# Kernel tuning notes

Hardware: AMD Instinct MI355X
Metric: run time of the kernel (lower is better)

## Reference

```python
import jax, jax.numpy as jnp
import numpy as np

L, B, E, H, NL = 512, 8, 1024, 16, 2
HD = E // H
DFF = 4 * E
EPS = 1e-5


def setup_inputs() -> dict:
    key = jax.random.key(0)
    ks = jax.random.split(key, 8)
    s = 0.02
    return {
        "src": jax.random.normal(ks[0], (L, B, E), jnp.float32),
        "position_embed": jax.random.normal(ks[1], (L, L, HD), jnp.float32) * s,
        "type_embed": jax.random.normal(ks[2], (L, L, HD), jnp.float32) * s,
        "Wi": jax.random.normal(ks[3], (NL, 3 * E, E), jnp.float32) * s,
        "bi": jnp.zeros((NL, 3 * E), jnp.float32),
        "Wo": jax.random.normal(ks[4], (NL, E, E), jnp.float32) * s,
        "bo": jnp.zeros((NL, E), jnp.float32),
        "W1": jax.random.normal(ks[5], (NL, DFF, E), jnp.float32) * s,
        "b1": jnp.zeros((NL, DFF), jnp.float32),
        "W2": jax.random.normal(ks[6], (NL, E, DFF), jnp.float32) * s,
        "b2": jnp.zeros((NL, E), jnp.float32),
        "g1": jnp.ones((NL, E), jnp.float32),
        "be1": jnp.zeros((NL, E), jnp.float32),
        "g2": jnp.ones((NL, E), jnp.float32),
        "be2": jnp.zeros((NL, E), jnp.float32),
    }


def _ln(x, g, b):
    m = jnp.mean(x, -1, keepdims=True)
    v = jnp.mean((x - m) ** 2, -1, keepdims=True)
    return (x - m) * jax.lax.rsqrt(v + EPS) * g + b


def _attn(src, pos, typ, Wi, bi, Wo, bo):
    # src: [L, B, E]
    p = src @ Wi.T + bi                      # [L, B, 3E]
    q, k, v = jnp.split(p, 3, axis=-1)
    q = q * (HD ** -0.5)
    # -> [B, H, L, HD]
    def hsplit(t):
        return t.reshape(L, B, H, HD).transpose(1, 2, 0, 3)
    q, k, v = hsplit(q), hsplit(k), hsplit(v)
    # scores = q k^T + type_embed@q + q@pos^T  (Shaw relative attention)
    scores = jnp.einsum('bhld,bhsd->bhls', q, k)
    scores = scores + jnp.einsum('bhld,lsd->bhls', q, pos)      # position term
    scores = scores + jnp.einsum('lsd,bhld->bhls', typ, q)      # type term
    w = jax.nn.softmax(scores, axis=-1)                          # [B, H, L, S]
    # output = w v + w@pos + typ^T@w
    out = jnp.einsum('bhls,bhsd->bhld', w, v)
    out = out + jnp.einsum('bhls,lsd->bhld', w, pos)
    out = out + jnp.einsum('bhls,lsd->bhld', w, typ)
    out = out.transpose(2, 0, 1, 3).reshape(L, B, E)            # [L, B, E]
    return out @ Wo.T + bo


def _layer(src, pos, typ, Wi, bi, Wo, bo, W1, b1, W2, b2, g1, be1, g2, be2):
    src2 = _attn(src, pos, typ, Wi, bi, Wo, bo)
    src = _ln(src + src2, g1, be1)
    h = jax.nn.gelu(src @ W1.T + b1, approximate=False)
    src2 = h @ W2.T + b2
    return _ln(src + src2, g2, be2)


def reference(src, position_embed, type_embed, Wi, bi, Wo, bo, W1, b1, W2, b2,
              g1, be1, g2, be2):
    out = src
    for i in range(NL):
        out = _layer(out, position_embed, type_embed,
                     Wi[i], bi[i], Wo[i], bo[i], W1[i], b1[i], W2[i], b2[i],
                     g1[i], be1[i], g2[i], be2[i])
    return out
```

## Files before the change

kernel.cpp:

```cpp
#include <hip/hip_runtime.h>
#include <hip/hip_bf16.h>
#include <math.h>


typedef __hip_bfloat16 bf16;
typedef short short8 __attribute__((ext_vector_type(8)));
typedef float f32x4 __attribute__((ext_vector_type(4)));

typedef __attribute__((address_space(1))) const void gvoid;
typedef __attribute__((address_space(3))) void lvoid;

constexpr int Lc = 512;
constexpr int Bc = 8;
constexpr int Ec = 1024;
constexpr int Hc = 16;
constexpr int HDc = 64;
constexpr int NLc = 2;
constexpr int DFFc = 4096;
constexpr int LB = Lc * Bc;
constexpr int BHc = Bc * Hc;
constexpr float EPSc = 1e-5f;

__device__ inline unsigned short f2bfu(float f) {
  union { __hip_bfloat16 h; unsigned short u; } cv;
  cv.h = __float2bfloat16(f);
  return cv.u;
}

template <bool ACC, bool GELU, bool OBF>
__global__ __launch_bounds__(256) void gemm_bt128d(
    int M, int N, int K,
    const bf16* __restrict__ A, int lda, long long sAz,
    const bf16* __restrict__ Bm, int ldb, long long sBz,
    void* __restrict__ Cv, int ldc, long long sCz,
    const float* __restrict__ bias) {
  __shared__ __align__(16) bf16 As[2 * 128 * 64];
  __shared__ __align__(16) bf16 Bs[2 * 128 * 64];
  const int tid = threadIdx.x;
  const int w = tid >> 6, lane = tid & 63, quad = lane >> 4, lr = lane & 15;
  const int wr = w >> 1, wc = w & 1;
  const int m0 = blockIdx.x * 128, n0 = blockIdx.y * 128;
  const long long z = blockIdx.z;
  A += z * sAz;
  Bm += z * sBz;
  float* Cf = (float*)Cv;
  bf16* Cb = (bf16*)Cv;

  f32x4 acc[4][4];
#pragma unroll
  for (int i = 0; i < 4; i++)
#pragma unroll
    for (int j = 0; j < 4; j++) acc[i][j] = {0.f, 0.f, 0.f, 0.f};

  const int rA = lane >> 3;
  const int cA = ((lane & 7) ^ (lane >> 3)) * 8;

  auto STAGE = [&](int buf, int kt) {
    const int k0 = kt << 6;
#pragma unroll
    for (int t = 0; t < 4; ++t) {
      const int chunk = w * 4 + t;
      const int row = chunk * 8 + rA;
      __builtin_amdgcn_global_load_lds(
          (gvoid*)(A + (long long)(m0 + row) * lda + k0 + cA),
          (lvoid*)(As + buf * 8192 + chunk * 512), 16, 0, 0);
      __builtin_amdgcn_global_load_lds(
          (gvoid*)(Bm + (long long)(n0 + row) * ldb + k0 + cA),
          (lvoid*)(Bs + buf * 8192 + chunk * 512), 16, 0, 0);
    }
  };

  auto LOAD = [&](int buf, short8 (&a)[2][4], short8 (&b)[2][4]) {
    const char* Ab = (const char*)(As + buf * 8192);
    const char* Bb = (const char*)(Bs + buf * 8192);
#pragma unroll
    for (int ks2 = 0; ks2 < 2; ks2++) {
      const int swzc = (ks2 * 64 + quad * 16) ^ ((lr & 7) << 4);
#pragma unroll
      for (int i = 0; i < 4; i++)
        a[ks2][i] = *(const short8*)(Ab + (wr * 64 + i * 16 + lr) * 128 + swzc);
#pragma unroll
      for (int j = 0; j < 4; j++)
        b[ks2][j] = *(const short8*)(Bb + (wc * 64 + j * 16 + lr) * 128 + swzc);
    }
  };

  auto MMA = [&](short8 (&a)[2][4], short8 (&b)[2][4]) {
#pragma unroll
    for (int ks2 = 0; ks2 < 2; ks2++)
#pragma unroll
      for (int i = 0; i < 4; i++)
#pragma unroll
        for (int j = 0; j < 4; j++)
          acc[i][j] = __builtin_amdgcn_mfma_f32_16x16x32_bf16(a[ks2][i], b[ks2][j], acc[i][j], 0, 0, 0);
  };

  const int nt = K >> 6;
  STAGE(0, 0);
  asm volatile("s_waitcnt vmcnt(0)" ::: "memory");
  __builtin_amdgcn_sched_barrier(0);
  __builtin_amdgcn_s_barrier();
  __builtin_amdgcn_sched_barrier(0);

  int cur = 0;
  for (int t = 0; t < nt - 1; ++t) {
    short8 a[2][4], b[2][4];
    LOAD(cur, a, b);
    __builtin_amdgcn_sched_barrier(0);
    STAGE(cur ^ 1, t + 1);
    __builtin_amdgcn_sched_barrier(0);
    __builtin_amdgcn_s_setprio(1);
    MMA(a, b);
    __builtin_amdgcn_s_setprio(0);
    asm volatile("s_waitcnt vmcnt(0)" ::: "memory");
    __builtin_amdgcn_sched_barrier(0);
    __builtin_amdgcn_s_barrier();
    __builtin_amdgcn_sched_barrier(0);
    cur ^= 1;
  }
  {
    short8 a[2][4], b[2][4];
    LOAD(cur, a, b);
    MMA(a, b);
  }

#pragma unroll
  for (int i = 0; i < 4; i++) {
#pragma unroll
    for (int j = 0; j < 4; j++) {
      int col = n0 + wc * 64 + j * 16 + lr;
      float bv = bias ? bias[col] : 0.f;
#pragma unroll
      for (int r = 0; r < 4; r++) {
        int row = m0 + wr * 64 + i * 16 + quad * 4 + r;
        long long off = z * sCz + (long long)row * ldc + col;
        float v = acc[i][j][r] + bv;
        if (ACC) v += Cf[off];
        if (GELU) v = 0.5f * v * (1.f + erff(v * 0.70710678118654752f));
        if (OBF)
          Cb[off] = __float2bfloat16(v);
        else
          Cf[off] = v;
      }
    }
  }
}

template <bool ACC, bool GELU, bool OBF>
__global__ __launch_bounds__(256) void gemm_bt(
    int M, int N, int K,
    const bf16* __restrict__ A, int lda, long long sAz,
    const bf16* __restrict__ Bm, int ldb, long long sBz,
    void* __restrict__ Cv, int ldc, long long sCz,
    const float* __restrict__ bias) {
  __shared__ __align__(16) bf16 As[128 * 72];
  __shared__ __align__(16) bf16 Bs[64 * 72];
  const int tid = threadIdx.x;
  const int w = tid >> 6, lane = tid & 63, quad = lane >> 4, lr = lane & 15;
  const int m0 = blockIdx.x * 128, n0 = blockIdx.y * 64;
  const long long z = blockIdx.z;
  A += z * sAz;
  Bm += z * sBz;
  float* Cf = (float*)Cv;
  bf16* Cb = (bf16*)Cv;

  f32x4 acc[2][4];
#pragma unroll
  for (int i = 0; i < 2; i++)
#pragma unroll
    for (int j = 0; j < 4; j++) acc[i][j] = {0.f, 0.f, 0.f, 0.f};

  for (int k0 = 0; k0 < K; k0 += 64) {
#pragma unroll
    for (int i = 0; i < 8; i++) {
      int slot = tid + i * 256;
      int r = slot >> 4, c4 = (slot & 15) << 2;
      const bf16* srcp = A + (long long)(m0 + r) * lda + k0 + c4;
      *(ushort4*)&As[r * 72 + c4] = *(const ushort4*)srcp;
    }
#pragma unroll
    for (int i = 0; i < 4; i++) {
      int slot = tid + i * 256;
      int r = slot >> 4, c4 = (slot & 15) << 2;
      const bf16* srcp = Bm + (long long)(n0 + r) * ldb + k0 + c4;
      *(ushort4*)&Bs[r * 72 + c4] = *(const ushort4*)srcp;
    }
    __syncthreads();
#pragma unroll
    for (int ks = 0; ks < 64; ks += 32) {
      short8 a[2], b[4];
#pragma unroll
      for (int i = 0; i < 2; i++)
        a[i] = *(const short8*)&As[(w * 32 + i * 16 + lr) * 72 + ks + quad * 8];
#pragma unroll
      for (int j = 0; j < 4; j++)
        b[j] = *(const short8*)&Bs[(j * 16 + lr) * 72 + ks + quad * 8];
#pragma unroll
      for (int i = 0; i < 2; i++)
#pragma unroll
        for (int j = 0; j < 4; j++)
          acc[i][j] = __builtin_amdgcn_mfma_f32_16x16x32_bf16(a[i], b[j], acc[i][j], 0, 0, 0);
    }
    __syncthreads();
  }

#pragma unroll
  for (int i = 0; i < 2; i++) {
#pragma unroll
    for (int j = 0; j < 4; j++) {
      int col = n0 + j * 16 + lr;
      float bv = bias ? bias[col] : 0.f;
#pragma unroll
      for (int r = 0; r < 4; r++) {
        int row = m0 + w * 32 + i * 16 + quad * 4 + r;
        long long off = z * sCz + (long long)row * ldc + col;
        float v = acc[i][j][r] + bv;
        if (ACC) v += Cf[off];
        if (GELU) v = 0.5f * v * (1.f + erff(v * 0.70710678118654752f));
        if (OBF)
          Cb[off] = __float2bfloat16(v);
        else
          Cf[off] = v;
      }
    }
  }
}

__global__ void cvt_bf16(const float* __restrict__ in, bf16* __restrict__ out, long long n) {
  long long i = (long long)blockIdx.x * 256 + threadIdx.x;
  if (i < n) out[i] = __float2bfloat16(in[i]);
}

__global__ void init_x(const float* __restrict__ src, float* __restrict__ x, bf16* __restrict__ xb) {
  long long i = (long long)blockIdx.x * 256 + threadIdx.x;
  float v = src[i];
  x[i] = v;
  xb[i] = __float2bfloat16(v);
}

__global__ void prep_R(const float* __restrict__ pos, const float* __restrict__ typ,
                       bf16* __restrict__ Rb, bf16* __restrict__ Rt) {
  __shared__ __align__(16) float Ls[64 * 68];
  int l = blockIdx.y, s0 = blockIdx.x * 64;
  int tid = threadIdx.x;
#pragma unroll
  for (int i = 0; i < 4; i++) {
    int slot = tid + i * 256;
    int r = slot >> 4, c = (slot & 15) << 2;
    long long off = (((long long)l) * Lc + s0 + r) * HDc + c;
    float4 a = *(const float4*)&pos[off];
    float4 b = *(const float4*)&typ[off];
    float4 s = {a.x + b.x, a.y + b.y, a.z + b.z, a.w + b.w};
    *(float4*)&Ls[r * 68 + c] = s;
    ushort4 o = {f2bfu(s.x), f2bfu(s.y), f2bfu(s.z), f2bfu(s.w)};
    *(ushort4*)&Rb[off] = o;
  }
  __syncthreads();
#pragma unroll
  for (int i = 0; i < 4; i++) {
    int slot = tid + i * 256;
    int d = slot >> 4, s4 = (slot & 15) << 2;
    ushort4 o = {f2bfu(Ls[(s4 + 0) * 68 + d]), f2bfu(Ls[(s4 + 1) * 68 + d]),
                 f2bfu(Ls[(s4 + 2) * 68 + d]), f2bfu(Ls[(s4 + 3) * 68 + d])};
    *(ushort4*)&Rt[(((long long)l) * HDc + d) * Lc + s0 + s4] = o;
  }
}

__global__ void split_qk(const float* __restrict__ P, bf16* __restrict__ q, bf16* __restrict__ k) {
  long long idx = (long long)blockIdx.x * 256 + threadIdx.x;
  int col = idx & (Ec - 1);
  long long row = idx >> 10;
  int l = (int)(row >> 3), b = (int)(row & 7);
  int h = col >> 6, d = col & 63;
  long long dst = (((long long)(b * Hc + h)) * Lc + l) * HDc + d;
  q[dst] = __float2bfloat16(P[row * 3072 + col] * 0.125f);
  k[dst] = __float2bfloat16(P[row * 3072 + Ec + col]);
}

__global__ void transpose_v(const float* __restrict__ P, bf16* __restrict__ vt) {
  __shared__ __align__(16) float Ls[64 * 68];
  int bh = blockIdx.y, b = bh >> 4, h = bh & 15;
  int l0 = blockIdx.x * 64;
  int tid = threadIdx.x;
#pragma unroll
  for (int i = 0; i < 4; i++) {
    int slot = tid + i * 256;
    int r = slot >> 4, c = (slot & 15) << 2;
    float4 v = *(const float4*)&P[((long long)(l0 + r) * Bc + b) * 3072 + 2 * Ec + h * 64 + c];
    *(float4*)&Ls[r * 68 + c] = v;
  }
  __syncthreads();
#pragma unroll
  for (int i = 0; i < 4; i++) {
    int slot = tid + i * 256;
    int d = slot >> 4, s4 = (slot & 15) << 2;
    ushort4 o = {f2bfu(Ls[(s4 + 0) * 68 + d]), f2bfu(Ls[(s4 + 1) * 68 + d]),
                 f2bfu(Ls[(s4 + 2) * 68 + d]), f2bfu(Ls[(s4 + 3) * 68 + d])};
    *(ushort4*)&vt[(((long long)(b * Hc + h)) * HDc + d) * Lc + l0 + s4] = o;
  }
}

__global__ __launch_bounds__(256) void softmax_rows(const float* S, bf16* P) {
  int w = threadIdx.x >> 6, lane = threadIdx.x & 63;
  long long row = (long long)blockIdx.x * 4 + w;
  const float* sr = S + row * 512;
  float4 v0 = *(const float4*)(sr + lane * 4);
  float4 v1 = *(const float4*)(sr + 256 + lane * 4);
  float mx = fmaxf(fmaxf(fmaxf(v0.x, v0.y), fmaxf(v0.z, v0.w)),
                   fmaxf(fmaxf(v1.x, v1.y), fmaxf(v1.z, v1.w)));
#pragma unroll
  for (int o = 32; o; o >>= 1) mx = fmaxf(mx, __shfl_xor(mx, o, 64));
  float e[8];
  e[0] = __expf(v0.x - mx); e[1] = __expf(v0.y - mx);
  e[2] = __expf(v0.z - mx); e[3] = __expf(v0.w - mx);
  e[4] = __expf(v1.x - mx); e[5] = __expf(v1.y - mx);
  e[6] = __expf(v1.z - mx); e[7] = __expf(v1.w - mx);
  float sum = e[0] + e[1] + e[2] + e[3] + e[4] + e[5] + e[6] + e[7];
#pragma unroll
  for (int o = 32; o; o >>= 1) sum += __shfl_xor(sum, o, 64);
  float inv = 1.f / sum;
  ushort4 o0 = {f2bfu(e[0] * inv), f2bfu(e[1] * inv), f2bfu(e[2] * inv), f2bfu(e[3] * inv)};
  ushort4 o1 = {f2bfu(e[4] * inv), f2bfu(e[5] * inv), f2bfu(e[6] * inv), f2bfu(e[7] * inv)};
  *(ushort4*)(P + row * 1024 + lane * 4) = o0;
  *(ushort4*)(P + row * 1024 + 256 + lane * 4) = o1;
}

__global__ void merge_ao(const float* __restrict__ ao2, bf16* __restrict__ aob) {
  long long i = (long long)blockIdx.x * 256 + threadIdx.x;
  int d = (int)(i & 63);
  long long t = i >> 6;
  int l = (int)(t & (Lc - 1));
  long long bh = t >> 9;
  int b = (int)(bh >> 4), h = (int)(bh & 15);
  aob[((long long)(l * Bc + b)) * Ec + h * 64 + d] = __float2bfloat16(ao2[i]);
}

__global__ __launch_bounds__(256) void add_ln4(
    const float* __restrict__ X, const float* __restrict__ Pp, long long pstride, int ns,
    const float* __restrict__ bias,
    const float* __restrict__ g, const float* __restrict__ be,
    float* __restrict__ outF, bf16* __restrict__ outB) {
  __shared__ float s_sum[4], s_sq[4];
  long long row = blockIdx.x;
  int tid = threadIdx.x;
  float4 xv = *(const float4*)&X[row * Ec + tid * 4];
  float4 bv = *(const float4*)&bias[tid * 4];
  float v[4] = {xv.x + bv.x, xv.y + bv.y, xv.z + bv.z, xv.w + bv.w};
  for (int s = 0; s < ns; ++s) {
    float4 pv = *(const float4*)&Pp[s * pstride + row * Ec + tid * 4];
    v[0] += pv.x; v[1] += pv.y; v[2] += pv.z; v[3] += pv.w;
  }
  float sm = v[0] + v[1] + v[2] + v[3];
  float sq = v[0] * v[0] + v[1] * v[1] + v[2] * v[2] + v[3] * v[3];
#pragma unroll
  for (int o = 32; o; o >>= 1) {
    sm += __shfl_xor(sm, o, 64);
    sq += __shfl_xor(sq, o, 64);
  }
  int w = tid >> 6, lane = tid & 63;
  if (lane == 0) {
    s_sum[w] = sm;
    s_sq[w] = sq;
  }
  __syncthreads();
  sm = s_sum[0] + s_sum[1] + s_sum[2] + s_sum[3];
  sq = s_sq[0] + s_sq[1] + s_sq[2] + s_sq[3];
  float mean = sm * (1.f / Ec);
  float var = sq * (1.f / Ec) - mean * mean;
  float rs = rsqrtf(var + EPSc);
#pragma unroll
  for (int e = 0; e < 4; e++) {
    int n = tid * 4 + e;
    float o = (v[e] - mean) * rs * g[n] + be[n];
    outF[row * Ec + n] = o;
    outB[row * Ec + n] = __float2bfloat16(o);
  }
}

static constexpr size_t WS_NEED = 327155712;

struct GlobalWs {
  void* p = nullptr;
  GlobalWs() {
    if (hipMalloc(&p, WS_NEED) != hipSuccess) p = nullptr;
  }
};
static GlobalWs g_ws;

extern "C" void kernel_launch(void* const* d_in, const int* in_sizes, int n_in,
                              void* d_out, int out_size, void* d_ws, size_t ws_size,
                              hipStream_t stream) {
  const float* src = (const float*)d_in[0];
  const float* pos = (const float*)d_in[1];
  const float* typ = (const float*)d_in[2];
  const float* Wi = (const float*)d_in[3];
  const float* bi = (const float*)d_in[4];
  const float* Wo = (const float*)d_in[5];
  const float* bo = (const float*)d_in[6];
  const float* W1 = (const float*)d_in[7];
  const float* b1 = (const float*)d_in[8];
  const float* W2 = (const float*)d_in[9];
  const float* b2 = (const float*)d_in[10];
  const float* g1 = (const float*)d_in[11];
  const float* be1 = (const float*)d_in[12];
  const float* g2 = (const float*)d_in[13];
  const float* be2 = (const float*)d_in[14];
  float* out = (float*)d_out;
  (void)in_sizes; (void)n_in; (void)out_size;

  char* wp = (ws_size >= WS_NEED) ? (char*)d_ws : (char*)g_ws.p;
  if (!wp) wp = (char*)d_ws;
  auto alloc = [&](size_t bytes) {
    char* r = wp;
    wp += (bytes + 255) & ~(size_t)255;
    return r;
  };

  char* U = alloc((size_t)BHc * Lc * Lc * 4);
  float* P = (float*)U;
  float* scores = (float*)U;
  bf16* probs = (bf16*)U;
  bf16* hb = (bf16*)U;
  float* part = (float*)(U + (size_t)34 * 1024 * 1024);
  const long long PSTRIDE = (long long)LB * Ec;

  float* x = (float*)alloc((size_t)LB * Ec * 4);
  bf16* xb = (bf16*)alloc((size_t)LB * Ec * 2);
  bf16* q = (bf16*)alloc((size_t)BHc * Lc * HDc * 2);
  bf16* k = (bf16*)alloc((size_t)BHc * Lc * HDc * 2);
  bf16* vt = (bf16*)alloc((size_t)BHc * HDc * Lc * 2);
  float* ao2 = (float*)alloc((size_t)BHc * Lc * HDc * 4);
  bf16* aob = (bf16*)alloc((size_t)LB * Ec * 2);
  bf16* Rb = (bf16*)alloc((size_t)Lc * Lc * HDc * 2);
  bf16* Rt = (bf16*)alloc((size_t)Lc * HDc * Lc * 2);
  bf16* wib = (bf16*)alloc((size_t)NLc * 3 * Ec * Ec * 2);
  bf16* wob = (bf16*)alloc((size_t)NLc * Ec * Ec * 2);
  bf16* w1b = (bf16*)alloc((size_t)NLc * DFFc * Ec * 2);
  bf16* w2b = (bf16*)alloc((size_t)NLc * Ec * DFFc * 2);

  {
    long long n;
    n = (long long)NLc * 3 * Ec * Ec;
    cvt_bf16<<<(int)((n + 255) / 256), 256, 0, stream>>>(Wi, wib, n);
    n = (long long)NLc * Ec * Ec;
    cvt_bf16<<<(int)((n + 255) / 256), 256, 0, stream>>>(Wo, wob, n);
    n = (long long)NLc * DFFc * Ec;
    cvt_bf16<<<(int)((n + 255) / 256), 256, 0, stream>>>(W1, w1b, n);
    n = (long long)NLc * Ec * DFFc;
    cvt_bf16<<<(int)((n + 255) / 256), 256, 0, stream>>>(W2, w2b, n);
  }
  prep_R<<<dim3(Lc / 64, Lc), 256, 0, stream>>>(pos, typ, Rb, Rt);
  init_x<<<LB * Ec / 256, 256, 0, stream>>>(src, x, xb);

  for (int i = 0; i < NLc; i++) {
    const bf16* Wi_b = wib + (size_t)i * 3 * Ec * Ec;
    const bf16* Wo_b = wob + (size_t)i * Ec * Ec;
    const bf16* W1_b = w1b + (size_t)i * DFFc * Ec;
    const bf16* W2_b = w2b + (size_t)i * Ec * DFFc;

    gemm_bt128d<false, false, false><<<dim3(LB / 128, 3 * Ec / 128, 1), 256, 0, stream>>>(
        LB, 3 * Ec, Ec, xb, Ec, 0, Wi_b, Ec, 0, P, 3 * Ec, 0, bi + (size_t)i * 3 * Ec);
    split_qk<<<LB * Ec / 256, 256, 0, stream>>>(P, q, k);
    transpose_v<<<dim3(Lc / 64, BHc), 256, 0, stream>>>(P, vt);

    gemm_bt<false, false, false><<<dim3(Lc / 128, Lc / 64, BHc), 256, 0, stream>>>(
        Lc, Lc, HDc, q, HDc, (long long)Lc * HDc, k, HDc, (long long)Lc * HDc,
        scores, Lc, (long long)Lc * Lc, nullptr);
    gemm_bt<true, false, false><<<dim3(1, Lc / 64, Lc), 256, 0, stream>>>(
        BHc, Lc, HDc, q, Lc * HDc, (long long)HDc, Rb, HDc, (long long)Lc * HDc,
        scores, Lc * Lc, (long long)Lc, nullptr);

    softmax_rows<<<BHc * Lc / 4, 256, 0, stream>>>(scores, probs);

    gemm_bt<false, false, false><<<dim3(Lc / 128, 1, BHc), 256, 0, stream>>>(
        Lc, HDc, Lc, probs, 1024, (long long)Lc * 1024, vt, Lc, (long long)HDc * Lc,
        ao2, HDc, (long long)Lc * HDc, nullptr);
    gemm_bt<true, false, false><<<dim3(1, 1, Lc), 256, 0, stream>>>(
        BHc, HDc, Lc, probs, Lc * 1024, (long long)1024, Rt, Lc, (long long)HDc * Lc,
        ao2, Lc * HDc, (long long)HDc, nullptr);

    merge_ao<<<BHc * Lc * HDc / 256, 256, 0, stream>>>(ao2, aob);

    gemm_bt128d<false, false, false><<<dim3(LB / 128, Ec / 128, 2), 256, 0, stream>>>(
        LB, Ec, Ec / 2, aob, Ec, (long long)(Ec / 2), Wo_b, Ec, (long long)(Ec / 2),
        part, Ec, PSTRIDE, nullptr);
    add_ln4<<<LB, 256, 0, stream>>>(x, part, PSTRIDE, 2, bo + (size_t)i * Ec,
                                    g1 + (size_t)i * Ec, be1 + (size_t)i * Ec, x, xb);

    gemm_bt128d<false, true, true><<<dim3(LB / 128, DFFc / 128, 1), 256, 0, stream>>>(
        LB, DFFc, Ec, xb, Ec, 0, W1_b, Ec, 0, hb, DFFc, 0, b1 + (size_t)i * DFFc);
    gemm_bt128d<false, false, false><<<dim3(LB / 128, Ec / 128, 2), 256, 0, stream>>>(
        LB, Ec, DFFc / 2, hb, DFFc, (long long)(DFFc / 2), W2_b, DFFc, (long long)(DFFc / 2),
        part, Ec, PSTRIDE, nullptr);

    float* outF = (i == NLc - 1) ? out : x;
    add_ln4<<<LB, 256, 0, stream>>>(x, part, PSTRIDE, 2, b2 + (size_t)i * Ec,
                                    g2 + (size_t)i * Ec, be2 + (size_t)i * Ec, outF, xb);
  }
}
```

Before: 1.097 ms.

## Fuse QK^T score GEMM into softmax kernel, reordering relative-term GEMM first

The separate q·k^T batched GEMM and the row softmax kernel are replaced by a single qk_softmax kernel. It computes the q·k^T tile with MFMA, adds the precomputed relative-position/type scores read from the scores buffer, and does the row max/sum reduction across four waves through shared memory before writing bf16 probabilities. The relative-term GEMM now writes (not accumulates) scores first. This removes one write plus re-read of the fp32 score tensor and one kernel launch. In exchange, q/k fragments are loaded straight from global memory without LDS staging, and extra block-level synchronisation is added.

```diff
diff --git a/kernel.cpp b/kernel.cpp
--- a/kernel.cpp
+++ b/kernel.cpp
@@ -5,6 +5,7 @@
 
 typedef __hip_bfloat16 bf16;
 typedef short short8 __attribute__((ext_vector_type(8)));
+typedef unsigned short ushort8 __attribute__((ext_vector_type(8)));
 typedef float f32x4 __attribute__((ext_vector_type(4)));
 
 typedef __attribute__((address_space(1))) const void gvoid;
@@ -226,6 +227,120 @@
   }
 }
 
+__global__ __launch_bounds__(256) void qk_softmax(
+    const bf16* __restrict__ q, const bf16* __restrict__ kk,
+    const float* S, bf16* Pr) {
+  __shared__ float red[4][32];
+  __shared__ __align__(16) unsigned short pbuf[32][520];
+  const int tid = threadIdx.x;
+  const int w = tid >> 6, lane = tid & 63, quad = lane >> 4, lr = lane & 15;
+  const int bh = blockIdx.z;
+  const int l0 = blockIdx.x * 32;
+  const int s0 = w * 128;
+  const long long qbase = (long long)bh * Lc * HDc;
+
+  f32x4 acc[2][8];
+#pragma unroll
+  for (int i = 0; i < 2; i++)
+#pragma unroll
+    for (int j = 0; j < 8; j++) acc[i][j] = {0.f, 0.f, 0.f, 0.f};
+
+#pragma unroll
+  for (int ks2 = 0; ks2 < 2; ks2++) {
+    short8 a[2], b[8];
+#pragma unroll
+    for (int i = 0; i < 2; i++)
+      a[i] = *(const short8*)&q[qbase + (long long)(l0 + i * 16 + lr) * HDc + ks2 * 32 + quad * 8];
+#pragma unroll
+    for (int j = 0; j < 8; j++)
+      b[j] = *(const short8*)&kk[qbase + (long long)(s0 + j * 16 + lr) * HDc + ks2 * 32 + quad * 8];
+#pragma unroll
+    for (int i = 0; i < 2; i++)
+#pragma unroll
+      for (int j = 0; j < 8; j++)
+        acc[i][j] = __builtin_amdgcn_mfma_f32_16x16x32_bf16(a[i], b[j], acc[i][j], 0, 0, 0);
+  }
+
+  const long long srow0 = (long long)bh * Lc + l0;
+#pragma unroll
+  for (int i = 0; i < 2; i++)
+#pragma unroll
+    for (int r = 0; r < 4; r++) {
+      const float* sp = S + (srow0 + i * 16 + quad * 4 + r) * Lc + s0 + lr;
+#pragma unroll
+      for (int j = 0; j < 8; j++) acc[i][j][r] += sp[j * 16];
+    }
+
+  float mx[2][4];
+#pragma unroll
+  for (int i = 0; i < 2; i++)
+#pragma unroll
+    for (int r = 0; r < 4; r++) {
+      float m = acc[i][0][r];
+#pragma unroll
+      for (int j = 1; j < 8; j++) m = fmaxf(m, acc[i][j][r]);
+#pragma unroll
+      for (int o = 8; o; o >>= 1) m = fmaxf(m, __shfl_xor(m, o, 64));
+      mx[i][r] = m;
+    }
+  if (lr == 0) {
+#pragma unroll
+    for (int i = 0; i < 2; i++)
+#pragma unroll
+      for (int r = 0; r < 4; r++) red[w][i * 16 + quad * 4 + r] = mx[i][r];
+  }
+  __syncthreads();
+#pragma unroll
+  for (int i = 0; i < 2; i++)
+#pragma unroll
+    for (int r = 0; r < 4; r++) {
+      int rr = i * 16 + quad * 4 + r;
+      mx[i][r] = fmaxf(fmaxf(red[0][rr], red[1][rr]), fmaxf(red[2][rr], red[3][rr]));
+    }
+  float sm[2][4];
+#pragma unroll
+  for (int i = 0; i < 2; i++)
+#pragma unroll
+    for (int r = 0; r < 4; r++) {
+      float s = 0.f;
+#pragma unroll
+      for (int j = 0; j < 8; j++) {
+        float e = __expf(acc[i][j][r] - mx[i][r]);
+        acc[i][j][r] = e;
+        s += e;
+      }
+#pragma unroll
+      for (int o = 8; o; o >>= 1) s += __shfl_xor(s, o, 64);
+      sm[i][r] = s;
+    }
+  __syncthreads();
+  if (lr == 0) {
+#pragma unroll
+    for (int i = 0; i < 2; i++)
+#pragma unroll
+      for (int r = 0; r < 4; r++) red[w][i * 16 + quad * 4 + r] = sm[i][r];
+  }
+  __syncthreads();
+#pragma unroll
+  for (int i = 0; i < 2; i++)
+#pragma unroll
+    for (int r = 0; r < 4; r++) {
+      int rr = i * 16 + quad * 4 + r;
+      float inv = 1.f / (red[0][rr] + red[1][rr] + red[2][rr] + red[3][rr]);
+#pragma unroll
+      for (int j = 0; j < 8; j++)
+        pbuf[rr][s0 + j * 16 + lr] = f2bfu(acc[i][j][r] * inv);
+    }
+  __syncthreads();
+#pragma unroll
+  for (int it = 0; it < 8; it++) {
+    int slot = tid + it * 256;
+    int row = slot >> 6, c8 = (slot & 63) * 8;
+    ushort8 v = *(const ushort8*)&pbuf[row][c8];
+    *(ushort8*)(Pr + (srow0 + row) * 1024 + c8) = v;
+  }
+}
+
 __global__ void cvt_bf16(const float* __restrict__ in, bf16* __restrict__ out, long long n) {
   long long i = (long long)blockIdx.x * 256 + threadIdx.x;
   if (i < n) out[i] = __float2bfloat16(in[i]);
@@ -298,31 +413,6 @@
                  f2bfu(Ls[(s4 + 2) * 68 + d]), f2bfu(Ls[(s4 + 3) * 68 + d])};
     *(ushort4*)&vt[(((long long)(b * Hc + h)) * HDc + d) * Lc + l0 + s4] = o;
   }
-}
-
-__global__ __launch_bounds__(256) void softmax_rows(const float* S, bf16* P) {
-  int w = threadIdx.x >> 6, lane = threadIdx.x & 63;
-  long long row = (long long)blockIdx.x * 4 + w;
-  const float* sr = S + row * 512;
-  float4 v0 = *(const float4*)(sr + lane * 4);
-  float4 v1 = *(const float4*)(sr + 256 + lane * 4);
-  float mx = fmaxf(fmaxf(fmaxf(v0.x, v0.y), fmaxf(v0.z, v0.w)),
-                   fmaxf(fmaxf(v1.x, v1.y), fmaxf(v1.z, v1.w)));
-#pragma unroll
-  for (int o = 32; o; o >>= 1) mx = fmaxf(mx, __shfl_xor(mx, o, 64));
-  float e[8];
-  e[0] = __expf(v0.x - mx); e[1] = __expf(v0.y - mx);
-  e[2] = __expf(v0.z - mx); e[3] = __expf(v0.w - mx);
-  e[4] = __expf(v1.x - mx); e[5] = __expf(v1.y - mx);
-  e[6] = __expf(v1.z - mx); e[7] = __expf(v1.w - mx);
-  float sum = e[0] + e[1] + e[2] + e[3] + e[4] + e[5] + e[6] + e[7];
-#pragma unroll
-  for (int o = 32; o; o >>= 1) sum += __shfl_xor(sum, o, 64);
-  float inv = 1.f / sum;
-  ushort4 o0 = {f2bfu(e[0] * inv), f2bfu(e[1] * inv), f2bfu(e[2] * inv), f2bfu(e[3] * inv)};
-  ushort4 o1 = {f2bfu(e[4] * inv), f2bfu(e[5] * inv), f2bfu(e[6] * inv), f2bfu(e[7] * inv)};
-  *(ushort4*)(P + row * 1024 + lane * 4) = o0;
-  *(ushort4*)(P + row * 1024 + 256 + lane * 4) = o1;
 }
 
 __global__ void merge_ao(const float* __restrict__ ao2, bf16* __restrict__ aob) {
@@ -463,14 +553,11 @@
     split_qk<<<LB * Ec / 256, 256, 0, stream>>>(P, q, k);
     transpose_v<<<dim3(Lc / 64, BHc), 256, 0, stream>>>(P, vt);
 
-    gemm_bt<false, false, false><<<dim3(Lc / 128, Lc / 64, BHc), 256, 0, stream>>>(
-        Lc, Lc, HDc, q, HDc, (long long)Lc * HDc, k, HDc, (long long)Lc * HDc,
-        scores, Lc, (long long)Lc * Lc, nullptr);
-    gemm_bt<true, false, false><<<dim3(1, Lc / 64, Lc), 256, 0, stream>>>(
+    gemm_bt<false, false, false><<<dim3(1, Lc / 64, Lc), 256, 0, stream>>>(
         BHc, Lc, HDc, q, Lc * HDc, (long long)HDc, Rb, HDc, (long long)Lc * HDc,
         scores, Lc * Lc, (long long)Lc, nullptr);
 
-    softmax_rows<<<BHc * Lc / 4, 256, 0, stream>>>(scores, probs);
+    qk_softmax<<<dim3(Lc / 32, 1, BHc), 256, 0, stream>>>(q, k, scores, probs);
 
     gemm_bt<false, false, false><<<dim3(Lc / 128, 1, BHc), 256, 0, stream>>>(
         Lc, HDc, Lc, probs, 1024, (long long)Lc * 1024, vt, Lc, (long long)HDc * Lc,
```

Result: faster. 1.017 ms (-7.3%).
